# Performance work log

Measured on AMD Instinct MI355X. Metric: run time of the kernel, lower is better.

Reference implementation:

```python
import jax, jax.numpy as jnp
import numpy as np

C = 256
EPS = 1e-5


def setup_inputs() -> dict:
    key = jax.random.key(0)
    ks = jax.random.split(key, 10)
    B, H, W = 4, 64, 64
    x1 = jax.random.normal(ks[0], (B, C, H, W), dtype=jnp.float32)
    x2 = jax.random.normal(ks[1], (B, C, H, W), dtype=jnp.float32)
    s = 1.0 / np.sqrt(C)
    qw = jax.random.normal(ks[2], (C, C), dtype=jnp.float32) * s
    qb = jax.random.normal(ks[3], (C,), dtype=jnp.float32) * 0.01
    kw = jax.random.normal(ks[4], (C, C), dtype=jnp.float32) * s
    kb = jax.random.normal(ks[5], (C,), dtype=jnp.float32) * 0.01
    vw = jax.random.normal(ks[6], (C, C), dtype=jnp.float32) * s
    vb = jax.random.normal(ks[7], (C,), dtype=jnp.float32) * 0.01
    ln_w = jnp.ones((C,), dtype=jnp.float32)
    ln_b = jnp.zeros((C,), dtype=jnp.float32)
    return {"x1": x1, "x2": x2, "qw": qw, "qb": qb, "kw": kw, "kb": kb,
            "vw": vw, "vb": vb, "ln_w": ln_w, "ln_b": ln_b}


def _conv1x1(x, w, b):
    # 1x1 conv == per-pixel matmul over channels. x: [B,C,H,W], w: [O,C]
    return jnp.einsum('oc,bchw->bohw', w, x) + b[None, :, None, None]


def reference(x1, x2, qw, qb, kw, kb, vw, vb, ln_w, ln_b):
    q = _conv1x1(x1, qw, qb)   # [B,C,H,W]
    k = _conv1x1(x2, kw, kb)   # [B,C,H,W]
    v = _conv1x1(x2, vw, vb)   # [B,C,H,W]
    # scores: [B,H,W,I,J]; softmax over LAST axis (j) only, as in the torch code
    scores = jnp.einsum('bchw,bcij->bhwij', q, k)
    attn = jax.nn.softmax(scores, axis=-1)
    fusion = jnp.einsum('bhwij,bcij->bchw', attn, v)  # [B,C,H,W]
    # LayerNorm2d: normalize over channel dim per spatial location
    mean = jnp.mean(fusion, axis=1, keepdims=True)
    var = jnp.var(fusion, axis=1, keepdims=True)
    normed = (fusion - mean) * jax.lax.rsqrt(var + EPS)
    return normed * ln_w[None, :, None, None] + ln_b[None, :, None, None]
```

## Files before the change

kernel.cpp:

```cpp
#include <hip/hip_runtime.h>


#define CDIM 256
#define NPOS 4096
#define BATCH 4
#define EPSV 1e-5f

typedef _Float16 f16;
typedef __attribute__((ext_vector_type(4))) _Float16 f16x4;
typedef __attribute__((ext_vector_type(8))) _Float16 f16x8;
typedef __attribute__((ext_vector_type(4))) float f32x4;
typedef __attribute__((ext_vector_type(16))) float f32x16;

#define WST       264
#define QK_STRIDE 264
#define V_STRIDE  72
#define DQ_STRIDE 72
#define F_STRIDE  68

#define LBAR() asm volatile("s_waitcnt lgkmcnt(0)\n\ts_barrier" ::: "memory")


static __device__ __forceinline__ f16x8 cvt8(const float* __restrict__ p) {
    float4 w0 = *(const float4*)p;
    float4 w1 = *(const float4*)(p + 4);
    f16x8 r;
    r[0] = (f16)w0.x; r[1] = (f16)w0.y; r[2] = (f16)w0.z; r[3] = (f16)w0.w;
    r[4] = (f16)w1.x; r[5] = (f16)w1.y; r[6] = (f16)w1.z; r[7] = (f16)w1.w;
    return r;
}

__global__ __launch_bounds__(256, 2) void gemm_kernel(
    const float* __restrict__ x1, const float* __restrict__ x2,
    const float* __restrict__ qw, const float* __restrict__ kw,
    const float* __restrict__ vw,
    const float* __restrict__ qb, const float* __restrict__ kb,
    const float* __restrict__ vb,
    f16* __restrict__ Qg, f16* __restrict__ Kg, f16* __restrict__ Vg)
{
    __shared__ f16 Xs[64 * WST];
    __shared__ f16 Wh[64 * WST];
    __shared__ f16 Ds[64 * DQ_STRIDE];
    __shared__ float biasS[256];

    const int id = blockIdx.x;
    const int pr  = id >> 8;
    const int rem = id & 255;
    const int b   = rem >> 6;
    const int p0  = (rem & 63) << 6;
    const float* xsrc = ((pr == 0) ? x1 : x2) + (size_t)b * CDIM * NPOS + p0;
    const float* Wfp  = (pr == 0) ? qw : (pr == 1) ? kw : vw;
    const float* bias = (pr == 0) ? qb : (pr == 1) ? kb : vb;

    const int t = threadIdx.x, w = t >> 6, l = t & 63, lm = l & 31, lh = l >> 5;
    const int pt = w & 1, ot = w >> 1;

    biasS[t] = bias[t];
    #pragma unroll
    for (int g = 0; g < 8; ++g) {
        f16x8 h;
        #pragma unroll
        for (int j = 0; j < 8; ++j)
            h[j] = (f16)xsrc[(size_t)(w * 64 + g * 8 + j) * NPOS + l];
        *(f16x8*)&Xs[l * WST + w * 64 + g * 8] = h;
    }

    for (int q = 0; q < 4; ++q) {
        #pragma unroll
        for (int i = 0; i < 8; ++i) {
            int g = t + i * 256;
            int row = g >> 5, col = (g & 31) * 8;
            *(f16x8*)&Wh[row * WST + col] =
                cvt8(Wfp + (size_t)(q * 64 + row) * CDIM + col);
        }
        __syncthreads();

        f32x16 accA = {}, accB = {};
        #pragma unroll
        for (int ks = 0; ks < 16; ks += 2) {
            f16x8 x0 = *(const f16x8*)&Xs[(pt * 32 + lm) * WST + ks * 16 + lh * 8];
            f16x8 w0 = *(const f16x8*)&Wh[(ot * 32 + lm) * WST + ks * 16 + lh * 8];
            f16x8 x1v = *(const f16x8*)&Xs[(pt * 32 + lm) * WST + (ks + 1) * 16 + lh * 8];
            f16x8 w1 = *(const f16x8*)&Wh[(ot * 32 + lm) * WST + (ks + 1) * 16 + lh * 8];
            if (pr < 2) {
                accA = __builtin_amdgcn_mfma_f32_32x32x16_f16(x0, w0, accA, 0, 0, 0);
                accB = __builtin_amdgcn_mfma_f32_32x32x16_f16(x1v, w1, accB, 0, 0, 0);
            } else {
                accA = __builtin_amdgcn_mfma_f32_32x32x16_f16(w0, x0, accA, 0, 0, 0);
                accB = __builtin_amdgcn_mfma_f32_32x32x16_f16(w1, x1v, accB, 0, 0, 0);
            }
        }

        if (pr < 2) {
            int o_l = ot * 32 + lm;
            float bv = biasS[q * 64 + o_l];
            #pragma unroll
            for (int r = 0; r < 16; ++r) {
                int p_l = pt * 32 + (r & 3) + 8 * (r >> 2) + 4 * lh;
                Ds[p_l * DQ_STRIDE + o_l] = (f16)(accA[r] + accB[r] + bv);
            }
        } else {
            #pragma unroll
            for (int r = 0; r < 16; ++r) {
                int o_l = ot * 32 + (r & 3) + 8 * (r >> 2) + 4 * lh;
                Ds[o_l * DQ_STRIDE + pt * 32 + lm] =
                    (f16)(accA[r] + accB[r] + biasS[q * 64 + o_l]);
            }
        }
        __syncthreads();

        #pragma unroll
        for (int j = 0; j < 2; ++j) {
            int row = (t >> 3) + j * 32;
            int cc  = (t & 7) * 8;
            f16x8 vdat = *(const f16x8*)&Ds[row * DQ_STRIDE + cc];
            if (pr < 2) {
                f16* Out = (pr == 0) ? Qg : Kg;
                *(f16x8*)(Out + ((size_t)(b * NPOS + p0 + row)) * CDIM + q * 64 + cc) = vdat;
            } else {
                *(f16x8*)(Vg + ((size_t)(b * CDIM + q * 64 + row)) * NPOS + p0 + cc) = vdat;
            }
        }
        __syncthreads();
    }
}

__global__ __launch_bounds__(256, 2) void attn_kernel(
    const f16* __restrict__ Qg, const f16* __restrict__ Kg, const f16* __restrict__ Vg,
    float* __restrict__ Fp)
{
    __shared__ f16   Ks[64 * QK_STRIDE];
    __shared__ f16   Vs[256 * V_STRIDE];
    __shared__ f16   Pl[64 * V_STRIDE];
    __shared__ float RedM[2][64], RedS[2][64];

    const int t    = threadIdx.x;
    const int L    = (int)((blockIdx.x & 7) * 64 + (blockIdx.x >> 3));
    const int grp  = L >> 6;
    const int b    = grp >> 1;
    const int half = grp & 1;
    const int qt   = L & 63;
    const int p0   = qt << 6;
    const int bq   = b * 64 + qt;
    const int w    = t >> 6;
    const int l    = t & 63;
    const int lm   = l & 31;
    const int lh   = l >> 5;
    const int spt  = w & 1;
    const int skt  = w >> 1;

    f16x8 qf[16];
    {
        const f16* qptr = Qg + (size_t)(b * NPOS + p0 + spt * 32 + lm) * CDIM + lh * 8;
        #pragma unroll
        for (int ks = 0; ks < 16; ++ks) qf[ks] = *(const f16x8*)(qptr + ks * 16);
    }

    const int kr = t >> 5, koff = (t & 31) * 8;
    f16x8 kreg[8];
    auto issue_k = [&](int ch) {
        const int i0 = ch * 64;
        #pragma unroll
        for (int r = 0; r < 8; ++r)
            kreg[r] = *(const f16x8*)(Kg + (size_t)(b * NPOS + i0 + r * 8 + kr) * CDIM + koff);
    };

    const int vr = t >> 3;
    const int vc = (t & 7) * 8;
    f16x8 vreg[8];
    auto issue_v = [&](int ch) {
        const int i0 = ch * 64;
        #pragma unroll
        for (int i = 0; i < 8; ++i)
            vreg[i] = *(const f16x8*)(Vg + (size_t)(b * CDIM + i * 32 + vr) * NPOS + i0 + vc);
    };

    issue_k(half * 32);
    issue_v(half * 32);

    f32x16 facc[4] = {};

    for (int it = 0; it < 32; ++it) {
        const int ch = half * 32 + it;

        #pragma unroll
        for (int r = 0; r < 8; ++r)
            *(f16x8*)&Ks[(r * 8 + kr) * QK_STRIDE + koff] = kreg[r];
        if (it < 31) issue_k(ch + 1);
        LBAR();

        #pragma unroll
        for (int i = 0; i < 8; ++i)
            *(f16x8*)&Vs[(i * 32 + vr) * V_STRIDE + vc] = vreg[i];
        if (it < 31) issue_v(ch + 1);

        f32x16 st = {};
        __builtin_amdgcn_s_setprio(1);
        #pragma unroll
        for (int ks = 0; ks < 16; ++ks) {
            f16x8 kf = *(const f16x8*)&Ks[(skt * 32 + lm) * QK_STRIDE + ks * 16 + lh * 8];
            st = __builtin_amdgcn_mfma_f32_32x32x16_f16(kf, qf[ks], st, 0, 0, 0);
        }
        __builtin_amdgcn_s_setprio(0);

        float mx = st[0];
        #pragma unroll
        for (int r = 1; r < 16; ++r) mx = fmaxf(mx, st[r]);
        mx = fmaxf(mx, __shfl_xor(mx, 32));
        float ss = 0.f;
        #pragma unroll
        for (int r = 0; r < 16; ++r) {
            float e = __expf(st[r] - mx);
            st[r] = e;
            ss += e;
        }
        ss += __shfl_xor(ss, 32);
        if (lh == 0) { RedM[skt][spt * 32 + lm] = mx; RedS[skt][spt * 32 + lm] = ss; }
        LBAR();

        float mo = RedM[skt ^ 1][spt * 32 + lm];
        float so = RedS[skt ^ 1][spt * 32 + lm];
        float M  = fmaxf(mx, mo);
        float S  = ss * __expf(mx - M) + so * __expf(mo - M);
        float scale = __expf(mx - M) * __builtin_amdgcn_rcpf(S);

        #pragma unroll
        for (int rq = 0; rq < 4; ++rq) {
            f16x4 pk;
            #pragma unroll
            for (int q2 = 0; q2 < 4; ++q2) pk[q2] = (f16)(st[rq * 4 + q2] * scale);
            *(f16x4*)&Pl[(spt * 32 + lm) * V_STRIDE + skt * 32 + rq * 8 + lh * 4] = pk;
        }
        LBAR();

        __builtin_amdgcn_s_setprio(1);
        #pragma unroll
        for (int kb = 0; kb < 4; ++kb) {
            f16x8 pf0 = *(const f16x8*)&Pl[lm * V_STRIDE + kb * 16 + lh * 8];
            f16x8 pf1 = *(const f16x8*)&Pl[(32 + lm) * V_STRIDE + kb * 16 + lh * 8];
            f16x8 va0 = *(const f16x8*)&Vs[(w * 64 + lm) * V_STRIDE + kb * 16 + lh * 8];
            f16x8 va1 = *(const f16x8*)&Vs[(w * 64 + 32 + lm) * V_STRIDE + kb * 16 + lh * 8];
            facc[0] = __builtin_amdgcn_mfma_f32_32x32x16_f16(va0, pf0, facc[0], 0, 0, 0);
            facc[1] = __builtin_amdgcn_mfma_f32_32x32x16_f16(va0, pf1, facc[1], 0, 0, 0);
            facc[2] = __builtin_amdgcn_mfma_f32_32x32x16_f16(va1, pf0, facc[2], 0, 0, 0);
            facc[3] = __builtin_amdgcn_mfma_f32_32x32x16_f16(va1, pf1, facc[3], 0, 0, 0);
        }
        __builtin_amdgcn_s_setprio(0);
    }

    float* dst = Fp + ((size_t)bq * 2 + half) * (CDIM * 64);
    #pragma unroll
    for (int ii = 0; ii < 2; ++ii)
        #pragma unroll
        for (int jj = 0; jj < 2; ++jj)
            #pragma unroll
            for (int r = 0; r < 16; ++r) {
                int c = w * 64 + ii * 32 + (r & 3) + 8 * (r >> 2) + 4 * lh;
                int p = jj * 32 + lm;
                dst[c * 64 + p] = facc[ii * 2 + jj][r];
            }
}

__global__ __launch_bounds__(256, 2) void merge_ln_kernel(
    const float* __restrict__ Fp, const float* __restrict__ ln_w,
    const float* __restrict__ ln_b, float* __restrict__ out)
{
    __shared__ float Fs[256 * F_STRIDE];
    __shared__ float redS[16 * 64], redQ[16 * 64];
    __shared__ float lnw_s[256], lnb_s[256];
    __shared__ float mu_s[64], rs_s[64];

    const int t  = threadIdx.x;
    const int bq = blockIdx.x;
    const int b  = bq >> 6;
    const int p0 = (bq & 63) << 6;

    lnw_s[t] = ln_w[t]; lnb_s[t] = ln_b[t];

    const int pb = (t & 15) * 4;
    const int cg = t >> 4;
    const float* base = Fp + (size_t)bq * 2 * (CDIM * 64);

    f32x4 s4 = {}, q4 = {};
    #pragma unroll 4
    for (int ci = 0; ci < 16; ++ci) {
        int c = cg * 16 + ci;
        size_t off = (size_t)c * 64 + pb;
        f32x4 v = *(const f32x4*)(base + off);
        v += *(const f32x4*)(base + (size_t)(CDIM * 64) + off);
        *(f32x4*)&Fs[c * F_STRIDE + pb] = v;
        s4 += v; q4 += v * v;
    }
    #pragma unroll
    for (int k2 = 0; k2 < 4; ++k2) {
        redS[cg * 64 + pb + k2] = s4[k2];
        redQ[cg * 64 + pb + k2] = q4[k2];
    }
    __syncthreads();
    if (t < 64) {
        float ss = 0.f, qq = 0.f;
        #pragma unroll
        for (int g2 = 0; g2 < 16; ++g2) { ss += redS[g2 * 64 + t]; qq += redQ[g2 * 64 + t]; }
        float mean = ss * (1.0f / 256.0f);
        float var  = qq * (1.0f / 256.0f) - mean * mean;
        mu_s[t] = mean;
        rs_s[t] = rsqrtf(var + EPSV);
    }
    __syncthreads();
    const int p   = t & 63;
    const int cg2 = t >> 6;
    const float mu = mu_s[p], rs = rs_s[p];
    float* dst = out + (size_t)b * CDIM * NPOS + p0 + p;
    #pragma unroll 4
    for (int ci = 0; ci < 64; ++ci) {
        int c = cg2 * 64 + ci;
        dst[(size_t)c * NPOS] = (Fs[c * F_STRIDE + p] - mu) * rs * lnw_s[c] + lnb_s[c];
    }
}

extern "C" void kernel_launch(void* const* d_in, const int* in_sizes, int n_in,
                              void* d_out, int out_size, void* d_ws, size_t ws_size,
                              hipStream_t stream)
{
    const float* x1  = (const float*)d_in[0];
    const float* x2  = (const float*)d_in[1];
    const float* qw  = (const float*)d_in[2];
    const float* qb  = (const float*)d_in[3];
    const float* kw  = (const float*)d_in[4];
    const float* kb  = (const float*)d_in[5];
    const float* vw  = (const float*)d_in[6];
    const float* vb  = (const float*)d_in[7];
    const float* lnw = (const float*)d_in[8];
    const float* lnb = (const float*)d_in[9];

    const size_t tsz = (size_t)BATCH * NPOS * CDIM;
    f16* Qg  = (f16*)d_ws;
    f16* Kg  = Qg + tsz;
    f16* Vg  = Kg + tsz;
    float* Fp = (float*)(Vg + tsz);

    gemm_kernel<<<768, 256, 0, stream>>>(x1, x2, qw, kw, vw, qb, kb, vb, Qg, Kg, Vg);
    attn_kernel<<<512, 256, 0, stream>>>(Qg, Kg, Vg, Fp);
    merge_ln_kernel<<<256, 256, 0, stream>>>(Fp, lnw, lnb, (float*)d_out);
}
```

Measured before the change: 218.5 us.

## Software-pipeline PV matmul with double-buffered P and direct V register loads

The attention kernel no longer stages V through shared memory. Each wave loads its V fragments straight from global memory into registers, and P is double-buffered so the previous chunk's PV MFMAs run between the softmax reduction and the next barrier. This removes one barrier per iteration and the V LDS traffic. Separately, the weights are converted to fp16 once in a new small kernel, and the GEMM prefetches the next weight slab into registers. The costs are an extra kernel launch, more VGPR pressure, and V global loads that are less coalesced.

New measurement: 222.8 us. No clear change (+2.0%).

```diff
diff --git a/kernel.cpp b/kernel.cpp
--- a/kernel.cpp
+++ b/kernel.cpp
@@ -14,7 +14,7 @@
 
 #define WST       264
 #define QK_STRIDE 264
-#define V_STRIDE  72
+#define P_STRIDE  72
 #define DQ_STRIDE 72
 #define F_STRIDE  68
 
@@ -30,10 +30,26 @@
     return r;
 }
 
+__global__ __launch_bounds__(256, 4) void wconv_kernel(
+    const float* __restrict__ qw, const float* __restrict__ kw,
+    const float* __restrict__ vw, f16* __restrict__ W16)
+{
+    const int id = blockIdx.x;
+    const int t  = threadIdx.x;
+    const int pr = id >> 2, h = id & 3;
+    const float* W = (pr == 0 ? qw : pr == 1 ? kw : vw) + (size_t)h * 64 * CDIM;
+    f16* D = W16 + (size_t)pr * CDIM * CDIM + (size_t)h * 64 * CDIM;
+    #pragma unroll
+    for (int i = 0; i < 8; ++i) {
+        int g = t + i * 256;
+        int row = g >> 5, col = (g & 31) * 8;
+        *(f16x8*)(D + (size_t)row * CDIM + col) = cvt8(W + (size_t)row * CDIM + col);
+    }
+}
+
 __global__ __launch_bounds__(256, 2) void gemm_kernel(
     const float* __restrict__ x1, const float* __restrict__ x2,
-    const float* __restrict__ qw, const float* __restrict__ kw,
-    const float* __restrict__ vw,
+    const f16* __restrict__ W16,
     const float* __restrict__ qb, const float* __restrict__ kb,
     const float* __restrict__ vb,
     f16* __restrict__ Qg, f16* __restrict__ Kg, f16* __restrict__ Vg)
@@ -49,11 +65,22 @@
     const int b   = rem >> 6;
     const int p0  = (rem & 63) << 6;
     const float* xsrc = ((pr == 0) ? x1 : x2) + (size_t)b * CDIM * NPOS + p0;
-    const float* Wfp  = (pr == 0) ? qw : (pr == 1) ? kw : vw;
+    const f16* Wp = W16 + (size_t)pr * CDIM * CDIM;
     const float* bias = (pr == 0) ? qb : (pr == 1) ? kb : vb;
 
     const int t = threadIdx.x, w = t >> 6, l = t & 63, lm = l & 31, lh = l >> 5;
     const int pt = w & 1, ot = w >> 1;
+
+    f16x8 wreg[8];
+    auto issue_w = [&](int q) {
+        #pragma unroll
+        for (int i = 0; i < 8; ++i) {
+            int g = t + i * 256;
+            int row = g >> 5, col = (g & 31) * 8;
+            wreg[i] = *(const f16x8*)(Wp + (size_t)(q * 64 + row) * CDIM + col);
+        }
+    };
+    issue_w(0);
 
     biasS[t] = bias[t];
     #pragma unroll
@@ -70,10 +97,10 @@
         for (int i = 0; i < 8; ++i) {
             int g = t + i * 256;
             int row = g >> 5, col = (g & 31) * 8;
-            *(f16x8*)&Wh[row * WST + col] =
-                cvt8(Wfp + (size_t)(q * 64 + row) * CDIM + col);
-        }
-        __syncthreads();
+            *(f16x8*)&Wh[row * WST + col] = wreg[i];
+        }
+        if (q < 3) issue_w(q + 1);
+        LBAR();
 
         f32x16 accA = {}, accB = {};
         #pragma unroll
@@ -107,7 +134,7 @@
                     (f16)(accA[r] + accB[r] + biasS[q * 64 + o_l]);
             }
         }
-        __syncthreads();
+        LBAR();
 
         #pragma unroll
         for (int j = 0; j < 2; ++j) {
@@ -121,7 +148,7 @@
                 *(f16x8*)(Vg + ((size_t)(b * CDIM + q * 64 + row)) * NPOS + p0 + cc) = vdat;
             }
         }
-        __syncthreads();
+        LBAR();
     }
 }
 
@@ -130,8 +157,7 @@
     float* __restrict__ Fp)
 {
     __shared__ f16   Ks[64 * QK_STRIDE];
-    __shared__ f16   Vs[256 * V_STRIDE];
-    __shared__ f16   Pl[64 * V_STRIDE];
+    __shared__ f16   Pl[2][64 * P_STRIDE];
     __shared__ float RedM[2][64], RedS[2][64];
 
     const int t    = threadIdx.x;
@@ -164,35 +190,23 @@
         for (int r = 0; r < 8; ++r)
             kreg[r] = *(const f16x8*)(Kg + (size_t)(b * NPOS + i0 + r * 8 + kr) * CDIM + koff);
     };
-
-    const int vr = t >> 3;
-    const int vc = (t & 7) * 8;
-    f16x8 vreg[8];
-    auto issue_v = [&](int ch) {
-        const int i0 = ch * 64;
-        #pragma unroll
-        for (int i = 0; i < 8; ++i)
-            vreg[i] = *(const f16x8*)(Vg + (size_t)(b * CDIM + i * 32 + vr) * NPOS + i0 + vc);
-    };
-
     issue_k(half * 32);
-    issue_v(half * 32);
+
+    const f16* vb0 = Vg + (size_t)(b * CDIM + w * 64 + lm) * NPOS;
+    const f16* vb1 = Vg + (size_t)(b * CDIM + w * 64 + 32 + lm) * NPOS;
+    f16x8 vfp0[4], vfp1[4];
 
     f32x16 facc[4] = {};
 
     for (int it = 0; it < 32; ++it) {
         const int ch = half * 32 + it;
+        const int pb = it & 1;
 
         #pragma unroll
         for (int r = 0; r < 8; ++r)
             *(f16x8*)&Ks[(r * 8 + kr) * QK_STRIDE + koff] = kreg[r];
         if (it < 31) issue_k(ch + 1);
         LBAR();
-
-        #pragma unroll
-        for (int i = 0; i < 8; ++i)
-            *(f16x8*)&Vs[(i * 32 + vr) * V_STRIDE + vc] = vreg[i];
-        if (it < 31) issue_v(ch + 1);
 
         f32x16 st = {};
         __builtin_amdgcn_s_setprio(1);
@@ -216,6 +230,29 @@
         }
         ss += __shfl_xor(ss, 32);
         if (lh == 0) { RedM[skt][spt * 32 + lm] = mx; RedS[skt][spt * 32 + lm] = ss; }
+
+        if (it > 0) {
+            const int pp = pb ^ 1;
+            __builtin_amdgcn_s_setprio(1);
+            #pragma unroll
+            for (int kb = 0; kb < 4; ++kb) {
+                f16x8 pf0 = *(const f16x8*)&Pl[pp][lm * P_STRIDE + kb * 16 + lh * 8];
+                f16x8 pf1 = *(const f16x8*)&Pl[pp][(32 + lm) * P_STRIDE + kb * 16 + lh * 8];
+                facc[0] = __builtin_amdgcn_mfma_f32_32x32x16_f16(vfp0[kb], pf0, facc[0], 0, 0, 0);
+                facc[1] = __builtin_amdgcn_mfma_f32_32x32x16_f16(vfp0[kb], pf1, facc[1], 0, 0, 0);
+                facc[2] = __builtin_amdgcn_mfma_f32_32x32x16_f16(vfp1[kb], pf0, facc[2], 0, 0, 0);
+                facc[3] = __builtin_amdgcn_mfma_f32_32x32x16_f16(vfp1[kb], pf1, facc[3], 0, 0, 0);
+            }
+            __builtin_amdgcn_s_setprio(0);
+        }
+        {
+            const int i0 = ch * 64;
+            #pragma unroll
+            for (int kb = 0; kb < 4; ++kb) {
+                vfp0[kb] = *(const f16x8*)(vb0 + i0 + kb * 16 + lh * 8);
+                vfp1[kb] = *(const f16x8*)(vb1 + i0 + kb * 16 + lh * 8);
+            }
+        }
         LBAR();
 
         float mo = RedM[skt ^ 1][spt * 32 + lm];
@@ -229,23 +266,22 @@
             f16x4 pk;
             #pragma unroll
             for (int q2 = 0; q2 < 4; ++q2) pk[q2] = (f16)(st[rq * 4 + q2] * scale);
-            *(f16x4*)&Pl[(spt * 32 + lm) * V_STRIDE + skt * 32 + rq * 8 + lh * 4] = pk;
-        }
-        LBAR();
-
-        __builtin_amdgcn_s_setprio(1);
+            *(f16x4*)&Pl[pb][(spt * 32 + lm) * P_STRIDE + skt * 32 + rq * 8 + lh * 4] = pk;
+        }
+    }
+
+    LBAR();
+    {
+        const int pp = 31 & 1;
         #pragma unroll
         for (int kb = 0; kb < 4; ++kb) {
-            f16x8 pf0 = *(const f16x8*)&Pl[lm * V_STRIDE + kb * 16 + lh * 8];
-            f16x8 pf1 = *(const f16x8*)&Pl[(32 + lm) * V_STRIDE + kb * 16 + lh * 8];
-            f16x8 va0 = *(const f16x8*)&Vs[(w * 64 + lm) * V_STRIDE + kb * 16 + lh * 8];
-            f16x8 va1 = *(const f16x8*)&Vs[(w * 64 + 32 + lm) * V_STRIDE + kb * 16 + lh * 8];
-            facc[0] = __builtin_amdgcn_mfma_f32_32x32x16_f16(va0, pf0, facc[0], 0, 0, 0);
-            facc[1] = __builtin_amdgcn_mfma_f32_32x32x16_f16(va0, pf1, facc[1], 0, 0, 0);
-            facc[2] = __builtin_amdgcn_mfma_f32_32x32x16_f16(va1, pf0, facc[2], 0, 0, 0);
-            facc[3] = __builtin_amdgcn_mfma_f32_32x32x16_f16(va1, pf1, facc[3], 0, 0, 0);
-        }
-        __builtin_amdgcn_s_setprio(0);
+            f16x8 pf0 = *(const f16x8*)&Pl[pp][lm * P_STRIDE + kb * 16 + lh * 8];
+            f16x8 pf1 = *(const f16x8*)&Pl[pp][(32 + lm) * P_STRIDE + kb * 16 + lh * 8];
+            facc[0] = __builtin_amdgcn_mfma_f32_32x32x16_f16(vfp0[kb], pf0, facc[0], 0, 0, 0);
+            facc[1] = __builtin_amdgcn_mfma_f32_32x32x16_f16(vfp0[kb], pf1, facc[1], 0, 0, 0);
+            facc[2] = __builtin_amdgcn_mfma_f32_32x32x16_f16(vfp1[kb], pf0, facc[2], 0, 0, 0);
+            facc[3] = __builtin_amdgcn_mfma_f32_32x32x16_f16(vfp1[kb], pf1, facc[3], 0, 0, 0);
+        }
     }
 
     float* dst = Fp + ((size_t)bq * 2 + half) * (CDIM * 64);
@@ -337,9 +373,11 @@
     f16* Qg  = (f16*)d_ws;
     f16* Kg  = Qg + tsz;
     f16* Vg  = Kg + tsz;
-    float* Fp = (float*)(Vg + tsz);
-
-    gemm_kernel<<<768, 256, 0, stream>>>(x1, x2, qw, kw, vw, qb, kb, vb, Qg, Kg, Vg);
+    f16* W16 = Vg + tsz;
+    float* Fp = (float*)(W16 + 3 * CDIM * CDIM);
+
+    wconv_kernel<<<12, 256, 0, stream>>>(qw, kw, vw, W16);
+    gemm_kernel<<<768, 256, 0, stream>>>(x1, x2, W16, qb, kb, vb, Qg, Kg, Vg);
     attn_kernel<<<512, 256, 0, stream>>>(Qg, Kg, Vg, Fp);
     merge_ln_kernel<<<256, 256, 0, stream>>>(Fp, lnw, lnb, (float*)d_out);
 }
```

## Pre-convert QKV weights to fp16 and prefetch weight tiles into registers

Applied to the files above, without the earlier changes.

A small kernel now converts the three fp32 weight matrices to fp16 once per call, so each of the 768 GEMM blocks reads half the weight bytes and skips the repeated conversion. Inside the GEMM, the next 64-row weight tile is loaded into registers while the current tile is being computed, which overlaps global loads with MFMA work. Block barriers become an LDS-only wait plus s_barrier. The cost is an extra kernel launch, extra workspace, and more register pressure from the prefetch buffer, which may affect occupancy at 2 blocks per CU.

Measured after the change: 215.0 us. No clear change (-1.6%).

```diff
diff --git a/kernel.cpp b/kernel.cpp
--- a/kernel.cpp
+++ b/kernel.cpp
@@ -30,10 +30,26 @@
     return r;
 }
 
+__global__ __launch_bounds__(256, 4) void wconv_kernel(
+    const float* __restrict__ qw, const float* __restrict__ kw,
+    const float* __restrict__ vw, f16* __restrict__ W16)
+{
+    const int id = blockIdx.x;
+    const int t  = threadIdx.x;
+    const int pr = id >> 2, h = id & 3;
+    const float* W = (pr == 0 ? qw : pr == 1 ? kw : vw) + (size_t)h * 64 * CDIM;
+    f16* D = W16 + (size_t)pr * CDIM * CDIM + (size_t)h * 64 * CDIM;
+    #pragma unroll
+    for (int i = 0; i < 8; ++i) {
+        int g = t + i * 256;
+        int row = g >> 5, col = (g & 31) * 8;
+        *(f16x8*)(D + (size_t)row * CDIM + col) = cvt8(W + (size_t)row * CDIM + col);
+    }
+}
+
 __global__ __launch_bounds__(256, 2) void gemm_kernel(
     const float* __restrict__ x1, const float* __restrict__ x2,
-    const float* __restrict__ qw, const float* __restrict__ kw,
-    const float* __restrict__ vw,
+    const f16* __restrict__ W16,
     const float* __restrict__ qb, const float* __restrict__ kb,
     const float* __restrict__ vb,
     f16* __restrict__ Qg, f16* __restrict__ Kg, f16* __restrict__ Vg)
@@ -49,11 +65,22 @@
     const int b   = rem >> 6;
     const int p0  = (rem & 63) << 6;
     const float* xsrc = ((pr == 0) ? x1 : x2) + (size_t)b * CDIM * NPOS + p0;
-    const float* Wfp  = (pr == 0) ? qw : (pr == 1) ? kw : vw;
+    const f16* Wp = W16 + (size_t)pr * CDIM * CDIM;
     const float* bias = (pr == 0) ? qb : (pr == 1) ? kb : vb;
 
     const int t = threadIdx.x, w = t >> 6, l = t & 63, lm = l & 31, lh = l >> 5;
     const int pt = w & 1, ot = w >> 1;
+
+    f16x8 wreg[8];
+    auto issue_w = [&](int q) {
+        #pragma unroll
+        for (int i = 0; i < 8; ++i) {
+            int g = t + i * 256;
+            int row = g >> 5, col = (g & 31) * 8;
+            wreg[i] = *(const f16x8*)(Wp + (size_t)(q * 64 + row) * CDIM + col);
+        }
+    };
+    issue_w(0);
 
     biasS[t] = bias[t];
     #pragma unroll
@@ -70,10 +97,10 @@
         for (int i = 0; i < 8; ++i) {
             int g = t + i * 256;
             int row = g >> 5, col = (g & 31) * 8;
-            *(f16x8*)&Wh[row * WST + col] =
-                cvt8(Wfp + (size_t)(q * 64 + row) * CDIM + col);
-        }
-        __syncthreads();
+            *(f16x8*)&Wh[row * WST + col] = wreg[i];
+        }
+        if (q < 3) issue_w(q + 1);
+        LBAR();
 
         f32x16 accA = {}, accB = {};
         #pragma unroll
@@ -107,7 +134,7 @@
                     (f16)(accA[r] + accB[r] + biasS[q * 64 + o_l]);
             }
         }
-        __syncthreads();
+        LBAR();
 
         #pragma unroll
         for (int j = 0; j < 2; ++j) {
@@ -121,7 +148,7 @@
                 *(f16x8*)(Vg + ((size_t)(b * CDIM + q * 64 + row)) * NPOS + p0 + cc) = vdat;
             }
         }
-        __syncthreads();
+        LBAR();
     }
 }
 
@@ -337,9 +364,11 @@
     f16* Qg  = (f16*)d_ws;
     f16* Kg  = Qg + tsz;
     f16* Vg  = Kg + tsz;
-    float* Fp = (float*)(Vg + tsz);
-
-    gemm_kernel<<<768, 256, 0, stream>>>(x1, x2, qw, kw, vw, qb, kb, vb, Qg, Kg, Vg);
+    f16* W16 = Vg + tsz;
+    float* Fp = (float*)(W16 + 3 * CDIM * CDIM);
+
+    wconv_kernel<<<12, 256, 0, stream>>>(qw, kw, vw, W16);
+    gemm_kernel<<<768, 256, 0, stream>>>(x1, x2, W16, qb, kb, vb, Qg, Kg, Vg);
     attn_kernel<<<512, 256, 0, stream>>>(Qg, Kg, Vg, Fp);
     merge_ln_kernel<<<256, 256, 0, stream>>>(Fp, lnw, lnb, (float*)d_out);
 }
```

## Pre-convert weights to fp16 MFMA fragment layout and load into registers

Applied to the files above, without the earlier changes.

Adds a small kernel that converts the Q/K/V weights to fp16 once per call, already arranged in the per-lane MFMA operand layout. The projection GEMM then loads weight fragments straight from global memory into registers, prefetching the next quarter during the epilogue, instead of staging fp32 weights through shared memory with a conversion and barrier each iteration. This removes the weight LDS buffer, which allows more blocks per CU. The cost is an extra kernel launch, more registers per thread, and redundant global weight reads across all blocks.

Measured after the change: 210.9 us. 3.5% less time.

```diff
diff --git a/kernel.cpp b/kernel.cpp
--- a/kernel.cpp
+++ b/kernel.cpp
@@ -30,16 +30,35 @@
     return r;
 }
 
-__global__ __launch_bounds__(256, 2) void gemm_kernel(
+__global__ __launch_bounds__(256, 4) void wconv_kernel(
+    const float* __restrict__ qw, const float* __restrict__ kw,
+    const float* __restrict__ vw, f16* __restrict__ Wf)
+{
+    const int id = blockIdx.x;
+    const int t  = threadIdx.x;
+    const int pr = id >> 3;
+    const int q  = (id >> 1) & 3;
+    const int ot = id & 1;
+    const float* W = (pr == 0 ? qw : pr == 1 ? kw : vw);
+    f16* D = Wf + (size_t)id * 8192;
+    #pragma unroll
+    for (int i = 0; i < 4; ++i) {
+        int idx = t + i * 256;
+        int ks = idx >> 6, l = idx & 63;
+        const float* src = W + (size_t)(q * 64 + ot * 32 + (l & 31)) * CDIM
+                             + ks * 16 + (l >> 5) * 8;
+        *(f16x8*)(D + (size_t)idx * 8) = cvt8(src);
+    }
+}
+
+__global__ __launch_bounds__(256, 3) void gemm_kernel(
     const float* __restrict__ x1, const float* __restrict__ x2,
-    const float* __restrict__ qw, const float* __restrict__ kw,
-    const float* __restrict__ vw,
+    const f16* __restrict__ Wf,
     const float* __restrict__ qb, const float* __restrict__ kb,
     const float* __restrict__ vb,
     f16* __restrict__ Qg, f16* __restrict__ Kg, f16* __restrict__ Vg)
 {
     __shared__ f16 Xs[64 * WST];
-    __shared__ f16 Wh[64 * WST];
     __shared__ f16 Ds[64 * DQ_STRIDE];
     __shared__ float biasS[256];
 
@@ -49,11 +68,12 @@
     const int b   = rem >> 6;
     const int p0  = (rem & 63) << 6;
     const float* xsrc = ((pr == 0) ? x1 : x2) + (size_t)b * CDIM * NPOS + p0;
-    const float* Wfp  = (pr == 0) ? qw : (pr == 1) ? kw : vw;
     const float* bias = (pr == 0) ? qb : (pr == 1) ? kb : vb;
 
     const int t = threadIdx.x, w = t >> 6, l = t & 63, lm = l & 31, lh = l >> 5;
     const int pt = w & 1, ot = w >> 1;
+
+    const f16* Wfp = Wf + (size_t)pr * 65536 + (size_t)ot * 8192;
 
     biasS[t] = bias[t];
     #pragma unroll
@@ -65,30 +85,33 @@
         *(f16x8*)&Xs[l * WST + w * 64 + g * 8] = h;
     }
 
+    f16x8 wf[16];
+    #pragma unroll
+    for (int ks = 0; ks < 16; ++ks)
+        wf[ks] = *(const f16x8*)(Wfp + (size_t)ks * 512 + l * 8);
+
+    __syncthreads();
+
     for (int q = 0; q < 4; ++q) {
-        #pragma unroll
-        for (int i = 0; i < 8; ++i) {
-            int g = t + i * 256;
-            int row = g >> 5, col = (g & 31) * 8;
-            *(f16x8*)&Wh[row * WST + col] =
-                cvt8(Wfp + (size_t)(q * 64 + row) * CDIM + col);
-        }
-        __syncthreads();
-
         f32x16 accA = {}, accB = {};
         #pragma unroll
         for (int ks = 0; ks < 16; ks += 2) {
-            f16x8 x0 = *(const f16x8*)&Xs[(pt * 32 + lm) * WST + ks * 16 + lh * 8];
-            f16x8 w0 = *(const f16x8*)&Wh[(ot * 32 + lm) * WST + ks * 16 + lh * 8];
+            f16x8 x0  = *(const f16x8*)&Xs[(pt * 32 + lm) * WST + ks * 16 + lh * 8];
             f16x8 x1v = *(const f16x8*)&Xs[(pt * 32 + lm) * WST + (ks + 1) * 16 + lh * 8];
-            f16x8 w1 = *(const f16x8*)&Wh[(ot * 32 + lm) * WST + (ks + 1) * 16 + lh * 8];
             if (pr < 2) {
-                accA = __builtin_amdgcn_mfma_f32_32x32x16_f16(x0, w0, accA, 0, 0, 0);
-                accB = __builtin_amdgcn_mfma_f32_32x32x16_f16(x1v, w1, accB, 0, 0, 0);
+                accA = __builtin_amdgcn_mfma_f32_32x32x16_f16(x0, wf[ks], accA, 0, 0, 0);
+                accB = __builtin_amdgcn_mfma_f32_32x32x16_f16(x1v, wf[ks + 1], accB, 0, 0, 0);
             } else {
-                accA = __builtin_amdgcn_mfma_f32_32x32x16_f16(w0, x0, accA, 0, 0, 0);
-                accB = __builtin_amdgcn_mfma_f32_32x32x16_f16(w1, x1v, accB, 0, 0, 0);
-            }
+                accA = __builtin_amdgcn_mfma_f32_32x32x16_f16(wf[ks], x0, accA, 0, 0, 0);
+                accB = __builtin_amdgcn_mfma_f32_32x32x16_f16(wf[ks + 1], x1v, accB, 0, 0, 0);
+            }
+        }
+
+        if (q < 3) {
+            #pragma unroll
+            for (int ks = 0; ks < 16; ++ks)
+                wf[ks] = *(const f16x8*)(Wfp + (size_t)(q + 1) * 16384
+                                             + (size_t)ks * 512 + l * 8);
         }
 
         if (pr < 2) {
@@ -107,7 +130,7 @@
                     (f16)(accA[r] + accB[r] + biasS[q * 64 + o_l]);
             }
         }
-        __syncthreads();
+        LBAR();
 
         #pragma unroll
         for (int j = 0; j < 2; ++j) {
@@ -121,7 +144,7 @@
                 *(f16x8*)(Vg + ((size_t)(b * CDIM + q * 64 + row)) * NPOS + p0 + cc) = vdat;
             }
         }
-        __syncthreads();
+        LBAR();
     }
 }
 
@@ -337,9 +360,11 @@
     f16* Qg  = (f16*)d_ws;
     f16* Kg  = Qg + tsz;
     f16* Vg  = Kg + tsz;
-    float* Fp = (float*)(Vg + tsz);
-
-    gemm_kernel<<<768, 256, 0, stream>>>(x1, x2, qw, kw, vw, qb, kb, vb, Qg, Kg, Vg);
+    f16* Wf  = Vg + tsz;
+    float* Fp = (float*)(Wf + 3 * CDIM * CDIM);
+
+    wconv_kernel<<<24, 256, 0, stream>>>(qw, kw, vw, Wf);
+    gemm_kernel<<<768, 256, 0, stream>>>(x1, x2, Wf, qb, kb, vb, Qg, Kg, Vg);
     attn_kernel<<<512, 256, 0, stream>>>(Qg, Kg, Vg, Fp);
     merge_ln_kernel<<<256, 256, 0, stream>>>(Fp, lnw, lnb, (float*)d_out);
 }
```
